# Kernel tuning notes

Hardware: AMD Instinct MI355X
Metric: run time of the kernel (lower is better)

Reference implementation:

```python
import jax, jax.numpy as jnp
import numpy as np

EMBED = 1024
HEADS = 16

def setup_inputs() -> dict:
    key = jax.random.key(0)
    k1, k2, k3, k4, k5 = jax.random.split(key, 5)
    x = jax.random.normal(k1, (2, 2048, EMBED), dtype=jnp.float32)
    s = 1.0 / np.sqrt(EMBED)
    W_atten = jax.random.normal(k2, (EMBED, 3 * EMBED), dtype=jnp.float32) * s
    b_atten = jax.random.normal(k3, (3 * EMBED,), dtype=jnp.float32) * 0.01
    W_proj = jax.random.normal(k4, (EMBED, EMBED), dtype=jnp.float32) * s
    b_proj = jax.random.normal(k5, (EMBED,), dtype=jnp.float32) * 0.01
    return {"x": x, "W_atten": W_atten, "b_atten": b_atten, "W_proj": W_proj, "b_proj": b_proj}

def reference(x, W_atten, b_atten, W_proj, b_proj):
    B, T, C = x.shape
    H = HEADS
    hs = C // H
    qkv = x @ W_atten + b_atten  # [B,T,3C]
    # NOTE: original splits as k, q, v (k first)
    k, q, v = jnp.split(qkv, 3, axis=2)
    k = k.reshape(B, T, H, hs).transpose(0, 2, 1, 3)  # [B,H,T,hs]
    q = q.reshape(B, T, H, hs).transpose(0, 2, 1, 3)
    v = v.reshape(B, T, H, hs).transpose(0, 2, 1, 3)
    scores = jnp.einsum('bhqd,bhkd->bhqk', q, k) / jnp.sqrt(jnp.float32(hs))
    causal = jnp.tril(jnp.ones((T, T), dtype=bool))
    scores = jnp.where(causal[None, None, :, :], scores, jnp.float32(-jnp.inf))
    att = jax.nn.softmax(scores, axis=-1)
    out = jnp.einsum('bhqk,bhkd->bhqd', att, v)  # [B,H,T,hs]
    out = out.transpose(0, 2, 1, 3).reshape(B, T, C)
    return out @ W_proj + b_proj
```

## Files before the change

### kernel.cpp

```cpp
#include <hip/hip_runtime.h>

typedef unsigned short u16;
typedef unsigned int u32;
typedef __bf16 bf16;
typedef bf16 bf16x8 __attribute__((ext_vector_type(8)));
typedef float f32x4 __attribute__((ext_vector_type(4)));
typedef u32 u32x4 __attribute__((ext_vector_type(4)));
typedef u16 u16x4 __attribute__((ext_vector_type(4)));

#define EMBED 1024
#define HEADS 16
#define HS 64
#define BATCH 2
#define SEQ 2048
#define M_TOT (BATCH * SEQ)
#define N_QKV (3 * EMBED)
#define KDIM  EMBED

#define CSCALE 0.18033688011112042f
#define MREF (64.0f * CSCALE)

__device__ __forceinline__ u16 f2bf(float f) {
  u32 u = __builtin_bit_cast(u32, f);
  u32 r = u + 0x7fffu + ((u >> 16) & 1u);
  return (u16)(r >> 16);
}
__device__ __forceinline__ float bf2f(u16 h) {
  return __builtin_bit_cast(float, (u32)h << 16);
}
__device__ __forceinline__ bf16x8 frag16(const u16* p) {
  return __builtin_bit_cast(bf16x8, *(const u32x4*)p);
}
__device__ __forceinline__ bf16x8 frag16u(const u32* p) {
  return __builtin_bit_cast(bf16x8, *(const u32x4*)p);
}
__device__ __forceinline__ float cl(float v) {
  return fminf(fmaxf(v, -3.0e4f), 3.0e4f);
}
__device__ __forceinline__ u32 pk2bf(float lo, float hi) {
  const u32 ul = __builtin_bit_cast(u32, lo) + 0x8000u;
  const u32 uh = __builtin_bit_cast(u32, hi) + 0x8000u;
  return (ul >> 16) | (uh & 0xFFFF0000u);
}

typedef __attribute__((address_space(1))) void gvoid;
typedef __attribute__((address_space(3))) void lvoid;
__device__ __forceinline__ void glds16(const u16* g, u16* l) {
  __builtin_amdgcn_global_load_lds((gvoid*)g, (lvoid*)l, 16, 0, 0);
}

__global__ __launch_bounds__(256) void convert_kernel(
    const float* __restrict__ in, u16* __restrict__ out, int n4) {
  const int i = blockIdx.x * 256 + threadIdx.x;
  if (i < n4) {
    f32x4 v = *(const f32x4*)(in + (size_t)i * 4);
    u16x4 pk;
#pragma unroll
    for (int j = 0; j < 4; j++) pk[j] = f2bf(v[j]);
    *(u16x4*)(out + (size_t)i * 4) = pk;
  }
}

__global__ __launch_bounds__(256) void transpose_conv_kernel(
    const float* __restrict__ in, u16* __restrict__ out, int R, int C) {
  __shared__ u16 tile[32][33];
  const int c0 = blockIdx.x * 32;
  const int r0 = blockIdx.y * 32;
  const int tx = threadIdx.x;
  const int ty = threadIdx.y;
#pragma unroll
  for (int i = 0; i < 32; i += 8)
    tile[ty + i][tx] = f2bf(in[(size_t)(r0 + ty + i) * C + c0 + tx]);
  __syncthreads();
#pragma unroll
  for (int i = 0; i < 32; i += 8)
    out[(size_t)(c0 + ty + i) * R + r0 + tx] = tile[tx][ty + i];
}

__global__ __launch_bounds__(256) void gemm_qkv_kernel(
    const u16* __restrict__ A, const u16* __restrict__ wt,
    const u16* __restrict__ bias, u16* __restrict__ kq, u16* __restrict__ vt) {
  __shared__ u16 As[128 * 32];
  __shared__ u16 Bs[128 * 32];
  const int tid = threadIdx.x;
  const int lane = tid & 63;
  const int wave = tid >> 6;
  const int quad = lane >> 4;
  const int l16 = lane & 15;
  const int wr = wave >> 1;
  const int wc = wave & 1;
  const int m0 = blockIdx.y * 128;
  const int n0 = blockIdx.x * 128;

  f32x4 acc[4][4] = {};
  const int grow = tid >> 2;
  const int gcol = (tid & 3) * 8;

  for (int k0 = 0; k0 < KDIM; k0 += 32) {
    __syncthreads();
    glds16(A + (size_t)(m0 + grow) * KDIM + k0 + gcol, As + tid * 8);
    glds16(A + (size_t)(m0 + grow + 64) * KDIM + k0 + gcol, As + 2048 + tid * 8);
    glds16(wt + (size_t)(n0 + grow) * KDIM + k0 + gcol, Bs + tid * 8);
    glds16(wt + (size_t)(n0 + grow + 64) * KDIM + k0 + gcol, Bs + 2048 + tid * 8);
    __syncthreads();

    bf16x8 af[4], bfr[4];
#pragma unroll
    for (int i = 0; i < 4; i++) {
      af[i]  = frag16(As + (wr * 64 + i * 16 + l16) * 32 + quad * 8);
      bfr[i] = frag16(Bs + (wc * 64 + i * 16 + l16) * 32 + quad * 8);
    }
#pragma unroll
    for (int mi = 0; mi < 4; mi++)
#pragma unroll
      for (int ni = 0; ni < 4; ni++)
        acc[mi][ni] = __builtin_amdgcn_mfma_f32_16x16x32_bf16(
            af[mi], bfr[ni], acc[mi][ni], 0, 0, 0);
  }

#pragma unroll
  for (int ni = 0; ni < 4; ni++) {
    const int n = n0 + wc * 64 + ni * 16 + l16;
    const float bv = bf2f(bias[n]);
    if (n < 2 * EMBED) {
#pragma unroll
      for (int mi = 0; mi < 4; mi++)
#pragma unroll
        for (int r = 0; r < 4; r++) {
          const int m = m0 + wr * 64 + mi * 16 + quad * 4 + r;
          kq[(size_t)m * 2048 + n] = f2bf(cl(acc[mi][ni][r] + bv));
        }
    } else {
      const int hd = n - 2 * EMBED;
#pragma unroll
      for (int mi = 0; mi < 4; mi++) {
        const int mbase = m0 + wr * 64 + mi * 16 + quad * 4;
        const int bqi = mbase >> 11;
        const int t0 = mbase & 2047;
        u16x4 pk;
#pragma unroll
        for (int r = 0; r < 4; r++) pk[r] = f2bf(cl(acc[mi][ni][r] + bv));
        *(u16x4*)(vt + ((size_t)bqi * EMBED + hd) * SEQ + t0) = pk;
      }
    }
  }
}

__global__ __launch_bounds__(128) void gemm_proj_kernel(
    const u16* __restrict__ A, const u16* __restrict__ wt,
    const u16* __restrict__ bias, float* __restrict__ out) {
  __shared__ u16 As[128 * 32];
  __shared__ u16 Bs[64 * 32];
  const int tid = threadIdx.x;
  const int lane = tid & 63;
  const int wave = tid >> 6;
  const int quad = lane >> 4;
  const int l16 = lane & 15;
  const int m0 = blockIdx.y * 128;
  const int n0 = blockIdx.x * 64;

  f32x4 acc[4][4] = {};
  const int grow = tid >> 2;
  const int gcol = (tid & 3) * 8;

  for (int k0 = 0; k0 < KDIM; k0 += 32) {
    __syncthreads();
#pragma unroll
    for (int p = 0; p < 4; p++)
      glds16(A + (size_t)(m0 + p * 32 + grow) * KDIM + k0 + gcol,
             As + p * 1024 + tid * 8);
#pragma unroll
    for (int p = 0; p < 2; p++)
      glds16(wt + (size_t)(n0 + p * 32 + grow) * KDIM + k0 + gcol,
             Bs + p * 1024 + tid * 8);
    __syncthreads();

    bf16x8 af[4], bfr[4];
#pragma unroll
    for (int i = 0; i < 4; i++) {
      af[i]  = frag16(As + (wave * 64 + i * 16 + l16) * 32 + quad * 8);
      bfr[i] = frag16(Bs + (i * 16 + l16) * 32 + quad * 8);
    }
#pragma unroll
    for (int mi = 0; mi < 4; mi++)
#pragma unroll
      for (int ni = 0; ni < 4; ni++)
        acc[mi][ni] = __builtin_amdgcn_mfma_f32_16x16x32_bf16(
            af[mi], bfr[ni], acc[mi][ni], 0, 0, 0);
  }

#pragma unroll
  for (int ni = 0; ni < 4; ni++) {
    const int n = n0 + ni * 16 + l16;
    const float bv = bf2f(bias[n]);
#pragma unroll
    for (int mi = 0; mi < 4; mi++)
#pragma unroll
      for (int r = 0; r < 4; r++) {
        const int m = m0 + wave * 64 + mi * 16 + quad * 4 + r;
        out[(size_t)m * EMBED + n] = cl(acc[mi][ni][r] + bv);
      }
  }
}

__global__ __launch_bounds__(128) void attn_kernel(
    const u16* __restrict__ kq, const u16* __restrict__ vt,
    u16* __restrict__ att) {
  __shared__ u16 Ks[2][64 * 64];
  __shared__ u32 Ps32[2][16 * 32];

  const int tid = threadIdx.x;
  const int lane = tid & 63;
  const int wave = tid >> 6;
  const int quad = lane >> 4;
  const int l16 = lane & 15;

  const int bh = blockIdx.x;
  const int qt32 = 63 - (int)blockIdx.y;
  const int q0 = qt32 * 32;
  const int bq = bh >> 4;
  const int h = bh & 15;

  const int q = q0 + wave * 16 + l16;
  const size_t qrow = (size_t)(bq * SEQ + q) * 2048 + EMBED + h * HS;
  bf16x8 bq0 = frag16(kq + qrow + quad * 8);
  bf16x8 bq1 = frag16(kq + qrow + 32 + quad * 8);

  const u16* kb = kq + (size_t)bq * SEQ * 2048 + h * HS;
  const u16* vb = vt + ((size_t)bq * EMBED + h * HS) * SEQ;
  u32* pw = Ps32[wave];
  const int psw32 = (l16 & 7) << 2;

  const int sw = quad ^ (l16 & 7);

  float lsum = 0.0f;
  f32x4 o[4] = {};

  const int nkt = (qt32 >> 1) + 1;
#pragma unroll
  for (int p = 0; p < 4; p++) {
    const int row = p * 16 + (tid >> 3);
    const int sgc = (tid & 7) ^ (row & 7);
    glds16(kb + (size_t)row * 2048 + sgc * 8, Ks[0] + row * 64 + (tid & 7) * 8);
  }

  for (int kt = 0; kt < nkt; kt++) {
    const int k0 = kt * 64;
    __syncthreads();
    if (kt + 1 < nkt) {
      const int kn = k0 + 64;
      u16* dst = Ks[(kt + 1) & 1];
#pragma unroll
      for (int p = 0; p < 4; p++) {
        const int row = p * 16 + (tid >> 3);
        const int sgc = (tid & 7) ^ (row & 7);
        glds16(kb + (size_t)(kn + row) * 2048 + sgc * 8, dst + row * 64 + (tid & 7) * 8);
      }
    }
    const u16* KsB = Ks[kt & 1];

    bf16x8 va[2][4];
#pragma unroll
    for (int kc = 0; kc < 2; kc++)
#pragma unroll
      for (int dc = 0; dc < 4; dc++)
        va[kc][dc] = frag16(vb + (size_t)(dc * 16 + l16) * SEQ + k0 + kc * 32 + quad * 8);

    f32x4 st[4] = {};
    __builtin_amdgcn_s_setprio(1);
#pragma unroll
    for (int sub = 0; sub < 4; sub++) {
      const u16* kr = KsB + (sub * 16 + l16) * 64;
      st[sub] = __builtin_amdgcn_mfma_f32_16x16x32_bf16(
          frag16(kr + sw * 8), bq0, st[sub], 0, 0, 0);
      st[sub] = __builtin_amdgcn_mfma_f32_16x16x32_bf16(
          frag16(kr + (sw ^ 4) * 8), bq1, st[sub], 0, 0, 0);
    }
    __builtin_amdgcn_s_setprio(0);

    float p[4][4];
    if (kt == nkt - 1) {
#pragma unroll
      for (int sub = 0; sub < 4; sub++)
#pragma unroll
        for (int r = 0; r < 4; r++) {
          const int key = k0 + sub * 16 + quad * 4 + r;
          const float e = __builtin_amdgcn_exp2f(st[sub][r] * CSCALE - MREF);
          p[sub][r] = (key <= q) ? e : 0.0f;
          lsum += p[sub][r];
        }
    } else {
#pragma unroll
      for (int sub = 0; sub < 4; sub++)
#pragma unroll
        for (int r = 0; r < 4; r++) {
          p[sub][r] = __builtin_amdgcn_exp2f(st[sub][r] * CSCALE - MREF);
          lsum += p[sub][r];
        }
    }

#pragma unroll
    for (int sub = 0; sub < 4; sub++)
#pragma unroll
      for (int rp = 0; rp < 2; rp++)
        pw[l16 * 32 + ((sub * 8 + quad * 2 + rp) ^ psw32)] =
            pk2bf(p[sub][2 * rp], p[sub][2 * rp + 1]);

#pragma unroll
    for (int kc = 0; kc < 2; kc++) {
      bf16x8 pb = frag16u(pw + l16 * 32 + ((kc * 16 + quad * 4) ^ psw32));
      __builtin_amdgcn_s_setprio(1);
#pragma unroll
      for (int dc = 0; dc < 4; dc++)
        o[dc] = __builtin_amdgcn_mfma_f32_16x16x32_bf16(va[kc][dc], pb, o[dc], 0, 0, 0);
      __builtin_amdgcn_s_setprio(0);
    }
  }

  lsum += __shfl_xor(lsum, 16);
  lsum += __shfl_xor(lsum, 32);

  const float inv = 1.0f / lsum;
  const size_t obase = (size_t)(bq * SEQ + q) * EMBED + h * HS;
#pragma unroll
  for (int dc = 0; dc < 4; dc++) {
    u16 sv[4];
#pragma unroll
    for (int r = 0; r < 4; r++) sv[r] = f2bf(cl(o[dc][r] * inv));
    *(u32*)(att + obase + dc * 16 + quad * 4) = (u32)sv[0] | ((u32)sv[1] << 16);
    *(u32*)(att + obase + dc * 16 + quad * 4 + 2) = (u32)sv[2] | ((u32)sv[3] << 16);
  }
}

extern "C" void kernel_launch(void* const* d_in, const int* in_sizes, int n_in,
                              void* d_out, int out_size, void* d_ws,
                              size_t ws_size, hipStream_t stream) {
  const float* x       = (const float*)d_in[0];
  const float* W_atten = (const float*)d_in[1];
  const float* b_atten = (const float*)d_in[2];
  const float* W_proj  = (const float*)d_in[3];
  const float* b_proj  = (const float*)d_in[4];

  u16* wt_a = (u16*)d_ws;
  u16* wt_p = wt_a + (size_t)N_QKV * EMBED;
  u16* ba   = wt_p + (size_t)EMBED * EMBED;
  u16* bp   = ba + N_QKV;
  u16* xb   = bp + EMBED;
  u16* kq   = xb + (size_t)M_TOT * KDIM;
  u16* vt   = kq + (size_t)M_TOT * 2048;
  u16* attb = xb;

  convert_kernel<<<(M_TOT * KDIM / 4 + 255) / 256, 256, 0, stream>>>(
      x, xb, M_TOT * KDIM / 4);
  convert_kernel<<<(N_QKV / 4 + 255) / 256, 256, 0, stream>>>(b_atten, ba, N_QKV / 4);
  convert_kernel<<<(EMBED / 4 + 255) / 256, 256, 0, stream>>>(b_proj, bp, EMBED / 4);
  transpose_conv_kernel<<<dim3(N_QKV / 32, EMBED / 32), dim3(32, 8), 0, stream>>>(
      W_atten, wt_a, EMBED, N_QKV);
  transpose_conv_kernel<<<dim3(EMBED / 32, EMBED / 32), dim3(32, 8), 0, stream>>>(
      W_proj, wt_p, EMBED, EMBED);
  gemm_qkv_kernel<<<dim3(N_QKV / 128, M_TOT / 128), 256, 0, stream>>>(
      xb, wt_a, ba, kq, vt);
  attn_kernel<<<dim3(BATCH * HEADS, SEQ / 32), 128, 0, stream>>>(kq, vt, attb);
  gemm_proj_kernel<<<dim3(EMBED / 64, M_TOT / 128), 128, 0, stream>>>(
      attb, wt_p, bp, (float*)d_out);
}
```

Before: 221.8 us.

## Process 64 query rows per attention block to reuse K and V tiles

Each attention block now covers two 32-row query groups (64 queries) instead of one. Every K tile read from shared memory and every V fragment loaded from global memory feeds MFMAs for both groups, and P is staged in a separate LDS buffer per group. This halves K/V traffic per query. In exchange the grid has half as many blocks and each thread keeps twice the accumulator and Q registers, which may lower occupancy and reduce load balance across the causal tiles.

```diff
diff --git a/kernel.cpp b/kernel.cpp
--- a/kernel.cpp
+++ b/kernel.cpp
@@ -207,7 +207,7 @@
     const u16* __restrict__ kq, const u16* __restrict__ vt,
     u16* __restrict__ att) {
   __shared__ u16 Ks[2][64 * 64];
-  __shared__ u32 Ps32[2][16 * 32];
+  __shared__ u32 Ps32[2][2][16 * 32];
 
   const int tid = threadIdx.x;
   const int lane = tid & 63;
@@ -216,27 +216,31 @@
   const int l16 = lane & 15;
 
   const int bh = blockIdx.x;
-  const int qt32 = 63 - (int)blockIdx.y;
-  const int q0 = qt32 * 32;
+  const int qt64 = 31 - (int)blockIdx.y;
+  const int q0 = qt64 * 64;
   const int bq = bh >> 4;
   const int h = bh & 15;
 
-  const int q = q0 + wave * 16 + l16;
-  const size_t qrow = (size_t)(bq * SEQ + q) * 2048 + EMBED + h * HS;
-  bf16x8 bq0 = frag16(kq + qrow + quad * 8);
-  bf16x8 bq1 = frag16(kq + qrow + 32 + quad * 8);
+  int qg[2];
+  bf16x8 bq0[2], bq1[2];
+#pragma unroll
+  for (int g = 0; g < 2; g++) {
+    qg[g] = q0 + g * 32 + wave * 16 + l16;
+    const size_t qrow = (size_t)(bq * SEQ + qg[g]) * 2048 + EMBED + h * HS;
+    bq0[g] = frag16(kq + qrow + quad * 8);
+    bq1[g] = frag16(kq + qrow + 32 + quad * 8);
+  }
 
   const u16* kb = kq + (size_t)bq * SEQ * 2048 + h * HS;
   const u16* vb = vt + ((size_t)bq * EMBED + h * HS) * SEQ;
-  u32* pw = Ps32[wave];
   const int psw32 = (l16 & 7) << 2;
 
   const int sw = quad ^ (l16 & 7);
 
-  float lsum = 0.0f;
-  f32x4 o[4] = {};
-
-  const int nkt = (qt32 >> 1) + 1;
+  float lsum[2] = {0.0f, 0.0f};
+  f32x4 o[2][4] = {};
+
+  const int nkt = qt64 + 1;
 #pragma unroll
   for (int p = 0; p < 4; p++) {
     const int row = p * 16 + (tid >> 3);
@@ -266,69 +270,86 @@
       for (int dc = 0; dc < 4; dc++)
         va[kc][dc] = frag16(vb + (size_t)(dc * 16 + l16) * SEQ + k0 + kc * 32 + quad * 8);
 
-    f32x4 st[4] = {};
+    f32x4 st[2][4] = {};
     __builtin_amdgcn_s_setprio(1);
 #pragma unroll
     for (int sub = 0; sub < 4; sub++) {
       const u16* kr = KsB + (sub * 16 + l16) * 64;
-      st[sub] = __builtin_amdgcn_mfma_f32_16x16x32_bf16(
-          frag16(kr + sw * 8), bq0, st[sub], 0, 0, 0);
-      st[sub] = __builtin_amdgcn_mfma_f32_16x16x32_bf16(
-          frag16(kr + (sw ^ 4) * 8), bq1, st[sub], 0, 0, 0);
+      const bf16x8 ka0 = frag16(kr + sw * 8);
+      const bf16x8 ka1 = frag16(kr + (sw ^ 4) * 8);
+#pragma unroll
+      for (int g = 0; g < 2; g++) {
+        st[g][sub] = __builtin_amdgcn_mfma_f32_16x16x32_bf16(
+            ka0, bq0[g], st[g][sub], 0, 0, 0);
+        st[g][sub] = __builtin_amdgcn_mfma_f32_16x16x32_bf16(
+            ka1, bq1[g], st[g][sub], 0, 0, 0);
+      }
     }
     __builtin_amdgcn_s_setprio(0);
 
-    float p[4][4];
-    if (kt == nkt - 1) {
+    const bool diag = (kt == nkt - 1);
+#pragma unroll
+    for (int g = 0; g < 2; g++) {
+      float p[4][4];
+      if (diag) {
+#pragma unroll
+        for (int sub = 0; sub < 4; sub++)
+#pragma unroll
+          for (int r = 0; r < 4; r++) {
+            const int key = k0 + sub * 16 + quad * 4 + r;
+            const float e = __builtin_amdgcn_exp2f(st[g][sub][r] * CSCALE - MREF);
+            p[sub][r] = (key <= qg[g]) ? e : 0.0f;
+            lsum[g] += p[sub][r];
+          }
+      } else {
+#pragma unroll
+        for (int sub = 0; sub < 4; sub++)
+#pragma unroll
+          for (int r = 0; r < 4; r++) {
+            p[sub][r] = __builtin_amdgcn_exp2f(st[g][sub][r] * CSCALE - MREF);
+            lsum[g] += p[sub][r];
+          }
+      }
+      u32* pw = Ps32[wave][g];
 #pragma unroll
       for (int sub = 0; sub < 4; sub++)
 #pragma unroll
-        for (int r = 0; r < 4; r++) {
-          const int key = k0 + sub * 16 + quad * 4 + r;
-          const float e = __builtin_amdgcn_exp2f(st[sub][r] * CSCALE - MREF);
-          p[sub][r] = (key <= q) ? e : 0.0f;
-          lsum += p[sub][r];
-        }
-    } else {
-#pragma unroll
-      for (int sub = 0; sub < 4; sub++)
-#pragma unroll
-        for (int r = 0; r < 4; r++) {
-          p[sub][r] = __builtin_amdgcn_exp2f(st[sub][r] * CSCALE - MREF);
-          lsum += p[sub][r];
-        }
-    }
-
-#pragma unroll
-    for (int sub = 0; sub < 4; sub++)
-#pragma unroll
-      for (int rp = 0; rp < 2; rp++)
-        pw[l16 * 32 + ((sub * 8 + quad * 2 + rp) ^ psw32)] =
-            pk2bf(p[sub][2 * rp], p[sub][2 * rp + 1]);
-
-#pragma unroll
-    for (int kc = 0; kc < 2; kc++) {
-      bf16x8 pb = frag16u(pw + l16 * 32 + ((kc * 16 + quad * 4) ^ psw32));
-      __builtin_amdgcn_s_setprio(1);
-#pragma unroll
-      for (int dc = 0; dc < 4; dc++)
-        o[dc] = __builtin_amdgcn_mfma_f32_16x16x32_bf16(va[kc][dc], pb, o[dc], 0, 0, 0);
-      __builtin_amdgcn_s_setprio(0);
-    }
-  }
-
-  lsum += __shfl_xor(lsum, 16);
-  lsum += __shfl_xor(lsum, 32);
-
-  const float inv = 1.0f / lsum;
-  const size_t obase = (size_t)(bq * SEQ + q) * EMBED + h * HS;
-#pragma unroll
-  for (int dc = 0; dc < 4; dc++) {
-    u16 sv[4];
-#pragma unroll
-    for (int r = 0; r < 4; r++) sv[r] = f2bf(cl(o[dc][r] * inv));
-    *(u32*)(att + obase + dc * 16 + quad * 4) = (u32)sv[0] | ((u32)sv[1] << 16);
-    *(u32*)(att + obase + dc * 16 + quad * 4 + 2) = (u32)sv[2] | ((u32)sv[3] << 16);
+        for (int rp = 0; rp < 2; rp++)
+          pw[l16 * 32 + ((sub * 8 + quad * 2 + rp) ^ psw32)] =
+              pk2bf(p[sub][2 * rp], p[sub][2 * rp + 1]);
+    }
+
+#pragma unroll
+    for (int g = 0; g < 2; g++) {
+      u32* pw = Ps32[wave][g];
+#pragma unroll
+      for (int kc = 0; kc < 2; kc++) {
+        bf16x8 pb = frag16u(pw + l16 * 32 + ((kc * 16 + quad * 4) ^ psw32));
+        __builtin_amdgcn_s_setprio(1);
+#pragma unroll
+        for (int dc = 0; dc < 4; dc++)
+          o[g][dc] = __builtin_amdgcn_mfma_f32_16x16x32_bf16(
+              va[kc][dc], pb, o[g][dc], 0, 0, 0);
+        __builtin_amdgcn_s_setprio(0);
+      }
+    }
+  }
+
+#pragma unroll
+  for (int g = 0; g < 2; g++) {
+    float ls = lsum[g];
+    ls += __shfl_xor(ls, 16);
+    ls += __shfl_xor(ls, 32);
+    const float inv = 1.0f / ls;
+    const size_t obase = (size_t)(bq * SEQ + qg[g]) * EMBED + h * HS;
+#pragma unroll
+    for (int dc = 0; dc < 4; dc++) {
+      u16 sv[4];
+#pragma unroll
+      for (int r = 0; r < 4; r++) sv[r] = f2bf(cl(o[g][dc][r] * inv));
+      *(u32*)(att + obase + dc * 16 + quad * 4) = (u32)sv[0] | ((u32)sv[1] << 16);
+      *(u32*)(att + obase + dc * 16 + quad * 4 + 2) = (u32)sv[2] | ((u32)sv[3] << 16);
+    }
   }
 }
 
@@ -360,7 +381,7 @@
       W_proj, wt_p, EMBED, EMBED);
   gemm_qkv_kernel<<<dim3(N_QKV / 128, M_TOT / 128), 256, 0, stream>>>(
       xb, wt_a, ba, kq, vt);
-  attn_kernel<<<dim3(BATCH * HEADS, SEQ / 32), 128, 0, stream>>>(kq, vt, attb);
+  attn_kernel<<<dim3(BATCH * HEADS, SEQ / 64), 128, 0, stream>>>(kq, vt, attb);
   gemm_proj_kernel<<<dim3(EMBED / 64, M_TOT / 128), 128, 0, stream>>>(
       attb, wt_p, bp, (float*)d_out);
 }
```

New measurement: 207.5 us. 1.07x faster.
